# Kernel tuning notes

Hardware: AMD Instinct MI355X
Metric: run time of the kernel (lower is better)

The kernel has to match this reference:

```python
import jax, jax.numpy as jnp
import numpy as np

N = 100000   # active voxels (stride=1 -> output coords == input coords)
C_IN = 64
C_OUT = 64
K3 = 27      # 3x3x3 kernel offsets
M = 40000    # rulebook pairs per kernel offset
EPS = 1e-5


def setup_inputs() -> dict:
    key = jax.random.key(0)
    k1, k2, k3, k4 = jax.random.split(key, 4)
    x = jax.random.normal(k1, (N, C_IN), dtype=jnp.float32)
    # conv weights per kernel offset: [K3, inc, outc]
    W = jax.random.normal(k2, (K3, C_IN, C_OUT), dtype=jnp.float32) * 0.05
    gamma = jnp.ones((C_OUT,), dtype=jnp.float32)
    beta = jnp.zeros((C_OUT,), dtype=jnp.float32)
    # rulebook: for each offset k, M (input_idx, output_idx) pairs
    in_idx = jax.random.randint(k3, (K3, M), 0, N, dtype=jnp.int32)
    out_idx = jax.random.randint(k4, (K3, M), 0, N, dtype=jnp.int32)
    return {"x": x, "W": W, "gamma": gamma, "beta": beta,
            "in_idx": in_idx, "out_idx": out_idx}


def reference(x, W, gamma, beta, in_idx, out_idx):
    n_out = x.shape[0]  # stride=1: output voxel set == input voxel set
    # gather: [K3, M, C_IN]
    feat = x[in_idx]
    # batched GEMM over kernel offsets: [K3, M, C_OUT]
    contrib = jnp.einsum('kmi,kio->kmo', feat, W)
    # scatter-add into output voxels
    out = jnp.zeros((n_out, W.shape[2]), dtype=x.dtype)
    out = out.at[out_idx.reshape(-1)].add(contrib.reshape(-1, W.shape[2]))
    # BatchNorm over active points (training-mode batch stats, biased var)
    mean = jnp.mean(out, axis=0)
    var = jnp.mean(jnp.square(out - mean), axis=0)
    y = (out - mean) * jax.lax.rsqrt(var + EPS) * gamma + beta
    # ReLU
    return jnp.maximum(y, 0.0)
```

## Files before the change

kernel.cpp:

```cpp
#include <hip/hip_runtime.h>


#define N_VOX   100000
#define NPAD    100096
#define C_INCH  64
#define C_OUTCH 64
#define K3      27
#define M_PAIRS 40000
#define NPAIRS  (K3 * M_PAIRS)
#define BN_EPS  1e-5f
#define NBINS   (K3 * NPAD)
#define AUXMAX  184320
#define AUXCAP  (AUXMAX - 1)
#define ZROW    (N_VOX + AUXMAX - 1)
#define OVMAX   65536

#define OFF_WT     0u
#define OFF_STATS  221184u
#define OFF_CTRS   221696u
#define OFF_CNT    221760u
#define OFF_GINX   2924352u
#define OFF_IN1    13734720u
#define OFF_LIST   24545088u
#define OFF_OV     26019648u
#define OFF_XB     26543936u
#define WS_NEED    ((size_t)OFF_XB + (size_t)(N_VOX + AUXMAX) * 128u)

#define NB_WT 432
#define NB_XB 3125

typedef __attribute__((ext_vector_type(8))) short bf16x8;
typedef __attribute__((ext_vector_type(4))) float f32x4;

__device__ __forceinline__ short f2bf(float f) {
  unsigned u = __builtin_bit_cast(unsigned, f);
  u += 0x7FFFu + ((u >> 16) & 1u);
  return (short)(u >> 16);
}
__device__ __forceinline__ float bf2f(short s) {
  unsigned u = ((unsigned)(unsigned short)s) << 16;
  return __builtin_bit_cast(float, u);
}

__global__ __launch_bounds__(256) void init_kernel(const float* __restrict__ W,
                                                   const float* __restrict__ x,
                                                   short* __restrict__ wt,
                                                   short* __restrict__ xb) {
  int b = blockIdx.x, t = threadIdx.x;
  if (b < NB_WT) {
    int id = b * 256 + t;
    int k = id >> 12, rem = id & 4095, c = rem >> 6, i = rem & 63;
    wt[id] = f2bf(W[(k << 12) + (i << 6) + c]);
  } else if (b < NB_WT + NB_XB) {
    int id = (b - NB_WT) * 256 + t;
    if (id < N_VOX * 8) {
      float4 lo = ((const float4*)x)[id * 2];
      float4 hi = ((const float4*)x)[id * 2 + 1];
      bf16x8 v;
      v[0] = f2bf(lo.x); v[1] = f2bf(lo.y); v[2] = f2bf(lo.z); v[3] = f2bf(lo.w);
      v[4] = f2bf(hi.x); v[5] = f2bf(hi.y); v[6] = f2bf(hi.z); v[7] = f2bf(hi.w);
      ((bf16x8*)xb)[id] = v;
    }
  } else {
    if (t < 8) {
      bf16x8 z = {0, 0, 0, 0, 0, 0, 0, 0};
      ((bf16x8*)(xb + (size_t)ZROW * 64))[t] = z;
    }
  }
}

__global__ __launch_bounds__(256) void build_kernel(const int* __restrict__ in_idx,
                                                    const int* __restrict__ out_idx,
                                                    unsigned* __restrict__ cnt32,
                                                    int* __restrict__ ginx,
                                                    int* __restrict__ in1,
                                                    int2* __restrict__ ov,
                                                    int* __restrict__ ctrs) {
  __shared__ int l_cnt, l_base;
  int t = threadIdx.x;
  if (t == 0) l_cnt = 0;
  __syncthreads();
  int id = blockIdx.x * 256 + t;
  int lpos = -1;
  int2 entry = make_int2(0, 0);
  if (id < NPAIRS) {
    int k  = id / M_PAIRS;
    int in = in_idx[id];
    int o  = out_idx[id];
    int b  = k * NPAD + o;
    unsigned sh   = (unsigned)(b & 3) * 8u;
    unsigned old  = atomicAdd(&cnt32[b >> 2], 1u << sh);
    unsigned slot = (old >> sh) & 0xFFu;
    if (slot == 0u)      ginx[b] = in;
    else if (slot == 1u) in1[b]  = in;
    else { lpos = atomicAdd(&l_cnt, 1); entry = make_int2((k << 17) | in, o); }
  }
  __syncthreads();
  if (t == 0) l_base = (l_cnt > 0) ? atomicAdd(&ctrs[1], l_cnt) : 0;
  __syncthreads();
  if (lpos >= 0) {
    int p = l_base + lpos;
    if (p < OVMAX) ov[p] = entry;
  }
}

__global__ __launch_bounds__(256) void scan_kernel(const unsigned* __restrict__ cnt32,
                                                   int* __restrict__ ginx,
                                                   const int* __restrict__ in1,
                                                   int2* __restrict__ list,
                                                   int* __restrict__ ctrs) {
  __shared__ int l_cnt, l_base;
  int t = threadIdx.x;
  if (t == 0) l_cnt = 0;
  __syncthreads();
  int w = blockIdx.x * 256 + t;
  unsigned c4 = (w < NBINS / 4) ? cnt32[w] : 0u;
  int lp[4];
  #pragma unroll
  for (int s = 0; s < 4; ++s) {
    unsigned c = (c4 >> (s * 8)) & 0xFFu;
    lp[s] = (c >= 2u) ? atomicAdd(&l_cnt, 1) : -1;
  }
  __syncthreads();
  if (t == 0) l_base = (l_cnt > 0) ? atomicAdd(&ctrs[0], l_cnt) : 0;
  __syncthreads();
  int base = l_base;
  #pragma unroll
  for (int s = 0; s < 4; ++s) {
    if (lp[s] >= 0) {
      int b   = w * 4 + s;
      int pos = base + lp[s];
      if (pos < AUXCAP) {
        list[pos] = make_int2(ginx[b], in1[b]);
        ginx[b]   = N_VOX + pos;
      }
    }
  }
}

__global__ __launch_bounds__(256) void fixup_kernel(short* __restrict__ xb,
                                                    const int2* __restrict__ list,
                                                    const int* __restrict__ ctrs) {
  int n = ctrs[0]; if (n > AUXCAP) n = AUXCAP;
  int wid  = (blockIdx.x * 256 + threadIdx.x) >> 6;
  int lane = threadIdx.x & 63;
  int nw   = gridDim.x * 4;
  for (int i = wid; i < n; i += nw) {
    int2 p = list[i];
    float a = bf2f(xb[(size_t)p.x * 64 + lane]);
    float b = bf2f(xb[(size_t)p.y * 64 + lane]);
    xb[(size_t)(N_VOX + i) * 64 + lane] = f2bf(a + b);
  }
}

__global__ __launch_bounds__(256) void conv_out_kernel(const short* __restrict__ xb,
                                                       const short* __restrict__ wt,
                                                       const int* __restrict__ ginx,
                                                       float* __restrict__ out) {
  __shared__ short lds[2 * 4096];
  int t = threadIdx.x, wave = t >> 6, lane = t & 63;
  int g = lane >> 4, c0 = lane & 15, g8 = g * 8;
  int obase = blockIdx.x * 64 + wave * 16;
  int o = obase + c0;

  int rb  = ((c0 * 128 + g * 16) ^ ((c0 & 7) << 4)) >> 1;
  int wb0 = ((t * 32) ^ (((t >> 2) & 7) << 4)) >> 1;

  f32x4 acc[4];
  #pragma unroll
  for (int n = 0; n < 4; ++n) { acc[n][0]=0.f; acc[n][1]=0.f; acc[n][2]=0.f; acc[n][3]=0.f; }

  bf16x8 s0 = *(const bf16x8*)(wt + t * 16);
  bf16x8 s1 = *(const bf16x8*)(wt + t * 16 + 8);
  int i0 = ginx[o];        i0 = (i0 < 0) ? ZROW : i0;
  const short* xr0 = xb + (size_t)i0 * 64;
  bf16x8 a0c = *(const bf16x8*)(xr0 + g8);
  bf16x8 a1c = *(const bf16x8*)(xr0 + 32 + g8);
  int i1 = ginx[NPAD + o]; i1 = (i1 < 0) ? ZROW : i1;
  *(bf16x8*)&lds[wb0]     = s0;
  *(bf16x8*)&lds[wb0 ^ 8] = s1;
  __syncthreads();

  int buf = 0;
  for (int k = 0; k < K3; ++k) {
    if (k + 1 < K3) {
      const short* wn = wt + (size_t)(k + 1) * 4096 + t * 16;
      s0 = *(const bf16x8*)(wn);
      s1 = *(const bf16x8*)(wn + 8);
    }
    const short* xr = xb + (size_t)i1 * 64;
    bf16x8 a0n = *(const bf16x8*)(xr + g8);
    bf16x8 a1n = *(const bf16x8*)(xr + 32 + g8);
    int i2 = ZROW;
    if (k + 2 < K3) { int r = ginx[(size_t)(k + 2) * NPAD + o]; i2 = (r < 0) ? ZROW : r; }

    const short* lb = lds + buf * 4096;
    #pragma unroll
    for (int n = 0; n < 4; ++n) {
      bf16x8 b0 = *(const bf16x8*)&lb[rb + n * 1024];
      bf16x8 b1 = *(const bf16x8*)&lb[(rb ^ 32) + n * 1024];
      acc[n] = __builtin_amdgcn_mfma_f32_16x16x32_bf16(a0c, b0, acc[n], 0, 0, 0);
      acc[n] = __builtin_amdgcn_mfma_f32_16x16x32_bf16(a1c, b1, acc[n], 0, 0, 0);
    }
    if (k + 1 < K3) {
      short* wd = lds + (buf ^ 1) * 4096;
      *(bf16x8*)&wd[wb0]     = s0;
      *(bf16x8*)&wd[wb0 ^ 8] = s1;
    }
    __syncthreads();
    a0c = a0n; a1c = a1n; i1 = i2; buf ^= 1;
  }

  int orow = obase + (g << 2);
  #pragma unroll
  for (int j = 0; j < 4; ++j) {
    int r = orow + j;
    if (r < N_VOX) {
      float* op = out + (size_t)r * 64 + c0;
      op[0]  = acc[0][j];
      op[16] = acc[1][j];
      op[32] = acc[2][j];
      op[48] = acc[3][j];
    }
  }
}

__global__ __launch_bounds__(256) void ov_kernel(const float* __restrict__ x,
                                                 const float* __restrict__ W,
                                                 const int2* __restrict__ ov,
                                                 const int* __restrict__ ctrs,
                                                 float* __restrict__ out) {
  int n = ctrs[1]; if (n > OVMAX) n = OVMAX;
  int wid  = (blockIdx.x * 256 + threadIdx.x) >> 6;
  int lane = threadIdx.x & 63;
  int nw   = gridDim.x * 4;
  for (int i = wid; i < n; i += nw) {
    int2 e = ov[i];
    int in = e.x & 0x1FFFF;
    int k  = e.x >> 17;
    int o  = e.y;
    const float* xr = x + (size_t)in * 64;
    const float* wp = W + (size_t)k * 4096 + lane;
    float d = 0.f;
    #pragma unroll 8
    for (int ii = 0; ii < 64; ++ii) d += xr[ii] * wp[ii * 64];
    unsafeAtomicAdd(&out[(size_t)o * 64 + lane], d);
  }
}

__global__ __launch_bounds__(256) void conv_kernel(const float* __restrict__ x,
                                                   const short* __restrict__ wt,
                                                   const int* __restrict__ in_idx,
                                                   const int* __restrict__ out_idx,
                                                   float* __restrict__ out) {
  __shared__ int s_in[64];
  __shared__ int s_out[64];
  int bx = blockIdx.x;
  int k = bx / (M_PAIRS / 64), base = (bx % (M_PAIRS / 64)) * 64;
  int t = threadIdx.x;
  if (t < 64)       s_in[t]       = in_idx[k * M_PAIRS + base + t];
  else if (t < 128) s_out[t - 64] = out_idx[k * M_PAIRS + base + (t - 64)];
  __syncthreads();
  int wave = t >> 6, lane = t & 63, g = lane >> 4, c0 = lane & 15;
  const float* xrow = x + (size_t)s_in[(wave << 4) + c0] * C_INCH + g * 8;
  float4 a0lo = *(const float4*)(xrow);
  float4 a0hi = *(const float4*)(xrow + 4);
  float4 a1lo = *(const float4*)(xrow + 32);
  float4 a1hi = *(const float4*)(xrow + 36);
  bf16x8 a0, a1;
  a0[0]=f2bf(a0lo.x); a0[1]=f2bf(a0lo.y); a0[2]=f2bf(a0lo.z); a0[3]=f2bf(a0lo.w);
  a0[4]=f2bf(a0hi.x); a0[5]=f2bf(a0hi.y); a0[6]=f2bf(a0hi.z); a0[7]=f2bf(a0hi.w);
  a1[0]=f2bf(a1lo.x); a1[1]=f2bf(a1lo.y); a1[2]=f2bf(a1lo.z); a1[3]=f2bf(a1lo.w);
  a1[4]=f2bf(a1hi.x); a1[5]=f2bf(a1hi.y); a1[6]=f2bf(a1hi.z); a1[7]=f2bf(a1hi.w);
  const short* wtk = wt + k * 4096;
  f32x4 acc[4];
  #pragma unroll
  for (int n = 0; n < 4; ++n) { acc[n][0]=0.f; acc[n][1]=0.f; acc[n][2]=0.f; acc[n][3]=0.f; }
  #pragma unroll
  for (int n = 0; n < 4; ++n) {
    int c = n * 16 + c0;
    bf16x8 b0 = *(const bf16x8*)(wtk + c * 64 + g * 8);
    bf16x8 b1 = *(const bf16x8*)(wtk + c * 64 + 32 + g * 8);
    acc[n] = __builtin_amdgcn_mfma_f32_16x16x32_bf16(a0, b0, acc[n], 0, 0, 0);
    acc[n] = __builtin_amdgcn_mfma_f32_16x16x32_bf16(a1, b1, acc[n], 0, 0, 0);
  }
  int rbase = (wave << 4) + ((lane >> 4) << 2);
  #pragma unroll
  for (int j = 0; j < 4; ++j) {
    size_t o2 = (size_t)s_out[rbase + j] * C_OUTCH;
    #pragma unroll
    for (int n = 0; n < 4; ++n) unsafeAtomicAdd(&out[o2 + n * 16 + c0], acc[n][j]);
  }
}

__global__ __launch_bounds__(256) void stats_kernel(const float* __restrict__ out,
                                                    float* __restrict__ stats) {
  __shared__ float s1[256], s2[256];
  int t = threadIdx.x, c = t & 63, rsub = t >> 6;
  float sum1 = 0.f, sum2 = 0.f;
  for (int r = blockIdx.x * 4 + rsub; r < N_VOX; r += gridDim.x * 4) {
    float v = out[r * 64 + c];
    sum1 += v; sum2 += v * v;
  }
  s1[t] = sum1; s2[t] = sum2;
  __syncthreads();
  if (t < 64) {
    sum1 = s1[t] + s1[t + 64] + s1[t + 128] + s1[t + 192];
    sum2 = s2[t] + s2[t + 64] + s2[t + 128] + s2[t + 192];
    unsafeAtomicAdd(&stats[c], sum1);
    unsafeAtomicAdd(&stats[64 + c], sum2);
  }
}

__global__ __launch_bounds__(256) void norm_kernel(float* __restrict__ out,
                                                   const float* __restrict__ stats,
                                                   const float* __restrict__ gamma,
                                                   const float* __restrict__ beta) {
  int i4 = blockIdx.x * 256 + threadIdx.x;
  if (i4 >= N_VOX * (C_OUTCH / 4)) return;
  const float invN = 1.0f / (float)N_VOX;
  float4 v = ((const float4*)out)[i4];
  int c0 = (i4 << 2) & 63;
  float r[4] = {v.x, v.y, v.z, v.w};
  #pragma unroll
  for (int j = 0; j < 4; ++j) {
    int c = c0 + j;
    float mean = stats[c] * invN;
    float ex2  = stats[64 + c] * invN;
    float var  = ex2 - mean * mean;
    float scale = gamma[c] * rsqrtf(var + BN_EPS);
    float shift = beta[c] - mean * scale;
    r[j] = fmaxf(r[j] * scale + shift, 0.0f);
  }
  v.x = r[0]; v.y = r[1]; v.z = r[2]; v.w = r[3];
  ((float4*)out)[i4] = v;
}

extern "C" void kernel_launch(void* const* d_in, const int* in_sizes, int n_in,
                              void* d_out, int out_size, void* d_ws, size_t ws_size,
                              hipStream_t stream) {
  const float* x      = (const float*)d_in[0];
  const float* W      = (const float*)d_in[1];
  const float* gamma  = (const float*)d_in[2];
  const float* beta   = (const float*)d_in[3];
  const int*   in_idx = (const int*)d_in[4];
  const int*   out_idx= (const int*)d_in[5];
  float* out = (float*)d_out;

  char* ws = (char*)d_ws;
  short*    wt    = (short*)(ws + OFF_WT);
  float*    stats = (float*)(ws + OFF_STATS);
  int*      ctrs  = (int*)(ws + OFF_CTRS);
  unsigned* cnt32 = (unsigned*)(ws + OFF_CNT);
  int*      ginx  = (int*)(ws + OFF_GINX);
  int*      in1   = (int*)(ws + OFF_IN1);
  int2*     list  = (int2*)(ws + OFF_LIST);
  int2*     ov    = (int2*)(ws + OFF_OV);
  short*    xb    = (short*)(ws + OFF_XB);

  hipMemsetAsync(ws + OFF_STATS, 0, OFF_CNT - OFF_STATS, stream);

  if (ws_size >= WS_NEED) {
    hipMemsetAsync(ws + OFF_CNT, 0x00, NBINS, stream);
    hipMemsetAsync(ws + OFF_GINX, 0xFF, NBINS * 4, stream);
    init_kernel<<<NB_WT + NB_XB + 1, 256, 0, stream>>>(W, x, wt, xb);
    build_kernel<<<(NPAIRS + 255) / 256, 256, 0, stream>>>(in_idx, out_idx,
                                                           cnt32, ginx, in1, ov, ctrs);
    scan_kernel<<<(NBINS / 4 + 255) / 256, 256, 0, stream>>>(cnt32, ginx, in1, list, ctrs);
    fixup_kernel<<<2048, 256, 0, stream>>>(xb, list, ctrs);
    conv_out_kernel<<<NPAD / 64, 256, 0, stream>>>(xb, wt, ginx, out);
    ov_kernel<<<1024, 256, 0, stream>>>(x, W, ov, ctrs, out);
  } else {
    init_kernel<<<NB_WT + NB_XB + 1, 256, 0, stream>>>(W, x, wt, xb);
    hipMemsetAsync(d_out, 0, (size_t)N_VOX * C_OUTCH * sizeof(float), stream);
    conv_kernel<<<K3 * (M_PAIRS / 64), 256, 0, stream>>>(x, wt, in_idx, out_idx, out);
  }

  stats_kernel<<<512, 256, 0, stream>>>(out, stats);
  norm_kernel<<<(N_VOX * (C_OUTCH / 4) + 255) / 256, 256, 0, stream>>>(out, stats, gamma, beta);
}
```

Baseline: 266.7 us.

## Replace count-based rulebook binning with linked lists and fuse BN stats into conv

Output-stationary binning now uses atomicExch-built linked lists per (offset, output) bin, so bins with any number of pairs are pre-summed in the fixup kernel. This removes the separate fp32 overflow kernel with its atomics, and the extra count and in1 arrays. The conv kernel now processes 128 outputs per block (two 16-row tiles per wave), reusing each LDS weight fragment across both tiles. It also accumulates BatchNorm sum and sum-of-squares directly, which drops the separate stats pass over the output. The cost is a fixup kernel that chases pointer chains, plus higher register pressure in conv.

```diff
diff --git a/kernel.cpp b/kernel.cpp
--- a/kernel.cpp
+++ b/kernel.cpp
@@ -13,17 +13,14 @@
 #define AUXMAX  184320
 #define AUXCAP  (AUXMAX - 1)
 #define ZROW    (N_VOX + AUXMAX - 1)
-#define OVMAX   65536
 
 #define OFF_WT     0u
 #define OFF_STATS  221184u
 #define OFF_CTRS   221696u
-#define OFF_CNT    221760u
-#define OFF_GINX   2924352u
-#define OFF_IN1    13734720u
-#define OFF_LIST   24545088u
-#define OFF_OV     26019648u
-#define OFF_XB     26543936u
+#define OFF_BING   221760u
+#define OFF_NODE   11032128u
+#define OFF_LIST   19672128u
+#define OFF_XB     20409472u
 #define WS_NEED    ((size_t)OFF_XB + (size_t)(N_VOX + AUXMAX) * 128u)
 
 #define NB_WT 432
@@ -71,181 +68,179 @@
 
 __global__ __launch_bounds__(256) void build_kernel(const int* __restrict__ in_idx,
                                                     const int* __restrict__ out_idx,
-                                                    unsigned* __restrict__ cnt32,
-                                                    int* __restrict__ ginx,
-                                                    int* __restrict__ in1,
-                                                    int2* __restrict__ ov,
-                                                    int* __restrict__ ctrs) {
+                                                    int* __restrict__ bing,
+                                                    int2* __restrict__ node) {
+  int id = blockIdx.x * 256 + threadIdx.x;
+  if (id >= NPAIRS) return;
+  int k  = id / M_PAIRS;
+  int in = in_idx[id];
+  int o  = out_idx[id];
+  int b  = k * NPAD + o;
+  int old = atomicExch(&bing[b], id);
+  node[id] = make_int2(old, in);
+}
+
+__global__ __launch_bounds__(256) void compact_kernel(int* __restrict__ bing,
+                                                      const int2* __restrict__ node,
+                                                      int* __restrict__ list,
+                                                      int* __restrict__ ctrs) {
   __shared__ int l_cnt, l_base;
   int t = threadIdx.x;
   if (t == 0) l_cnt = 0;
   __syncthreads();
-  int id = blockIdx.x * 256 + t;
-  int lpos = -1;
-  int2 entry = make_int2(0, 0);
-  if (id < NPAIRS) {
-    int k  = id / M_PAIRS;
-    int in = in_idx[id];
-    int o  = out_idx[id];
-    int b  = k * NPAD + o;
-    unsigned sh   = (unsigned)(b & 3) * 8u;
-    unsigned old  = atomicAdd(&cnt32[b >> 2], 1u << sh);
-    unsigned slot = (old >> sh) & 0xFFu;
-    if (slot == 0u)      ginx[b] = in;
-    else if (slot == 1u) in1[b]  = in;
-    else { lpos = atomicAdd(&l_cnt, 1); entry = make_int2((k << 17) | in, o); }
-  }
-  __syncthreads();
-  if (t == 0) l_base = (l_cnt > 0) ? atomicAdd(&ctrs[1], l_cnt) : 0;
-  __syncthreads();
-  if (lpos >= 0) {
-    int p = l_base + lpos;
-    if (p < OVMAX) ov[p] = entry;
-  }
-}
-
-__global__ __launch_bounds__(256) void scan_kernel(const unsigned* __restrict__ cnt32,
-                                                   int* __restrict__ ginx,
-                                                   const int* __restrict__ in1,
-                                                   int2* __restrict__ list,
-                                                   int* __restrict__ ctrs) {
-  __shared__ int l_cnt, l_base;
-  int t = threadIdx.x;
-  if (t == 0) l_cnt = 0;
-  __syncthreads();
   int w = blockIdx.x * 256 + t;
-  unsigned c4 = (w < NBINS / 4) ? cnt32[w] : 0u;
+  bool ok = (w < NBINS / 4);
+  int4 h4 = ok ? ((int4*)bing)[w] : make_int4(-1, -1, -1, -1);
+  int hv[4] = {h4.x, h4.y, h4.z, h4.w};
+  int gv[4];
   int lp[4];
+  int2 n0[4];
   #pragma unroll
   for (int s = 0; s < 4; ++s) {
-    unsigned c = (c4 >> (s * 8)) & 0xFFu;
-    lp[s] = (c >= 2u) ? atomicAdd(&l_cnt, 1) : -1;
+    lp[s] = -1;
+    if (hv[s] < 0) { gv[s] = ZROW; }
+    else {
+      n0[s] = node[hv[s]];
+      if (n0[s].x < 0) gv[s] = n0[s].y;
+      else             lp[s] = atomicAdd(&l_cnt, 1);
+    }
   }
   __syncthreads();
   if (t == 0) l_base = (l_cnt > 0) ? atomicAdd(&ctrs[0], l_cnt) : 0;
   __syncthreads();
-  int base = l_base;
   #pragma unroll
   for (int s = 0; s < 4; ++s) {
     if (lp[s] >= 0) {
-      int b   = w * 4 + s;
-      int pos = base + lp[s];
-      if (pos < AUXCAP) {
-        list[pos] = make_int2(ginx[b], in1[b]);
-        ginx[b]   = N_VOX + pos;
-      }
-    }
-  }
+      int pos = l_base + lp[s];
+      if (pos < AUXCAP) { list[pos] = hv[s]; gv[s] = N_VOX + pos; }
+      else              { gv[s] = n0[s].y; }
+    }
+  }
+  if (ok) ((int4*)bing)[w] = make_int4(gv[0], gv[1], gv[2], gv[3]);
 }
 
 __global__ __launch_bounds__(256) void fixup_kernel(short* __restrict__ xb,
-                                                    const int2* __restrict__ list,
+                                                    const int* __restrict__ list,
+                                                    const int2* __restrict__ node,
                                                     const int* __restrict__ ctrs) {
   int n = ctrs[0]; if (n > AUXCAP) n = AUXCAP;
   int wid  = (blockIdx.x * 256 + threadIdx.x) >> 6;
   int lane = threadIdx.x & 63;
   int nw   = gridDim.x * 4;
   for (int i = wid; i < n; i += nw) {
-    int2 p = list[i];
-    float a = bf2f(xb[(size_t)p.x * 64 + lane]);
-    float b = bf2f(xb[(size_t)p.y * 64 + lane]);
-    xb[(size_t)(N_VOX + i) * 64 + lane] = f2bf(a + b);
+    int h = list[i];
+    float acc = 0.f;
+    while (h >= 0) {
+      int2 nd = node[h];
+      acc += bf2f(xb[(size_t)nd.y * 64 + lane]);
+      h = nd.x;
+    }
+    xb[(size_t)(N_VOX + i) * 64 + lane] = f2bf(acc);
   }
 }
 
 __global__ __launch_bounds__(256) void conv_out_kernel(const short* __restrict__ xb,
                                                        const short* __restrict__ wt,
-                                                       const int* __restrict__ ginx,
-                                                       float* __restrict__ out) {
+                                                       const int* __restrict__ bing,
+                                                       float* __restrict__ out,
+                                                       float* __restrict__ stats) {
   __shared__ short lds[2 * 4096];
+  __shared__ float ls[128];
   int t = threadIdx.x, wave = t >> 6, lane = t & 63;
   int g = lane >> 4, c0 = lane & 15, g8 = g * 8;
-  int obase = blockIdx.x * 64 + wave * 16;
-  int o = obase + c0;
+  int o0 = blockIdx.x * 128 + wave * 32 + c0;
+  int o1 = o0 + 16;
 
   int rb  = ((c0 * 128 + g * 16) ^ ((c0 & 7) << 4)) >> 1;
   int wb0 = ((t * 32) ^ (((t >> 2) & 7) << 4)) >> 1;
-
-  f32x4 acc[4];
-  #pragma unroll
-  for (int n = 0; n < 4; ++n) { acc[n][0]=0.f; acc[n][1]=0.f; acc[n][2]=0.f; acc[n][3]=0.f; }
-
-  bf16x8 s0 = *(const bf16x8*)(wt + t * 16);
-  bf16x8 s1 = *(const bf16x8*)(wt + t * 16 + 8);
-  int i0 = ginx[o];        i0 = (i0 < 0) ? ZROW : i0;
-  const short* xr0 = xb + (size_t)i0 * 64;
-  bf16x8 a0c = *(const bf16x8*)(xr0 + g8);
-  bf16x8 a1c = *(const bf16x8*)(xr0 + 32 + g8);
-  int i1 = ginx[NPAD + o]; i1 = (i1 < 0) ? ZROW : i1;
-  *(bf16x8*)&lds[wb0]     = s0;
-  *(bf16x8*)&lds[wb0 ^ 8] = s1;
+  if (t < 128) ls[t] = 0.f;
+
+  f32x4 acc0[4], acc1[4];
+  #pragma unroll
+  for (int n = 0; n < 4; ++n) {
+    acc0[n][0]=0.f; acc0[n][1]=0.f; acc0[n][2]=0.f; acc0[n][3]=0.f;
+    acc1[n][0]=0.f; acc1[n][1]=0.f; acc1[n][2]=0.f; acc1[n][3]=0.f;
+  }
+
+  bf16x8 s0w = *(const bf16x8*)(wt + t * 16);
+  bf16x8 s1w = *(const bf16x8*)(wt + t * 16 + 8);
+  int ia = bing[o0], ib = bing[o1];
+  const short* xa = xb + (size_t)ia * 64;
+  const short* xc = xb + (size_t)ib * 64;
+  bf16x8 a0c = *(const bf16x8*)(xa + g8);
+  bf16x8 a1c = *(const bf16x8*)(xa + 32 + g8);
+  bf16x8 a2c = *(const bf16x8*)(xc + g8);
+  bf16x8 a3c = *(const bf16x8*)(xc + 32 + g8);
+  int i1a = bing[NPAD + o0], i1b = bing[NPAD + o1];
+  *(bf16x8*)&lds[wb0]     = s0w;
+  *(bf16x8*)&lds[wb0 ^ 8] = s1w;
   __syncthreads();
 
   int buf = 0;
   for (int k = 0; k < K3; ++k) {
     if (k + 1 < K3) {
       const short* wn = wt + (size_t)(k + 1) * 4096 + t * 16;
-      s0 = *(const bf16x8*)(wn);
-      s1 = *(const bf16x8*)(wn + 8);
-    }
-    const short* xr = xb + (size_t)i1 * 64;
-    bf16x8 a0n = *(const bf16x8*)(xr + g8);
-    bf16x8 a1n = *(const bf16x8*)(xr + 32 + g8);
-    int i2 = ZROW;
-    if (k + 2 < K3) { int r = ginx[(size_t)(k + 2) * NPAD + o]; i2 = (r < 0) ? ZROW : r; }
-
+      s0w = *(const bf16x8*)(wn);
+      s1w = *(const bf16x8*)(wn + 8);
+    }
+    const short* pa = xb + (size_t)i1a * 64;
+    const short* pb = xb + (size_t)i1b * 64;
+    bf16x8 a0n = *(const bf16x8*)(pa + g8);
+    bf16x8 a1n = *(const bf16x8*)(pa + 32 + g8);
+    bf16x8 a2n = *(const bf16x8*)(pb + g8);
+    bf16x8 a3n = *(const bf16x8*)(pb + 32 + g8);
+    int i2a = ZROW, i2b = ZROW;
+    if (k + 2 < K3) {
+      i2a = bing[(size_t)(k + 2) * NPAD + o0];
+      i2b = bing[(size_t)(k + 2) * NPAD + o1];
+    }
     const short* lb = lds + buf * 4096;
     #pragma unroll
     for (int n = 0; n < 4; ++n) {
       bf16x8 b0 = *(const bf16x8*)&lb[rb + n * 1024];
       bf16x8 b1 = *(const bf16x8*)&lb[(rb ^ 32) + n * 1024];
-      acc[n] = __builtin_amdgcn_mfma_f32_16x16x32_bf16(a0c, b0, acc[n], 0, 0, 0);
-      acc[n] = __builtin_amdgcn_mfma_f32_16x16x32_bf16(a1c, b1, acc[n], 0, 0, 0);
+      acc0[n] = __builtin_amdgcn_mfma_f32_16x16x32_bf16(a0c, b0, acc0[n], 0, 0, 0);
+      acc0[n] = __builtin_amdgcn_mfma_f32_16x16x32_bf16(a1c, b1, acc0[n], 0, 0, 0);
+      acc1[n] = __builtin_amdgcn_mfma_f32_16x16x32_bf16(a2c, b0, acc1[n], 0, 0, 0);
+      acc1[n] = __builtin_amdgcn_mfma_f32_16x16x32_bf16(a3c, b1, acc1[n], 0, 0, 0);
     }
     if (k + 1 < K3) {
       short* wd = lds + (buf ^ 1) * 4096;
-      *(bf16x8*)&wd[wb0]     = s0;
-      *(bf16x8*)&wd[wb0 ^ 8] = s1;
+      *(bf16x8*)&wd[wb0]     = s0w;
+      *(bf16x8*)&wd[wb0 ^ 8] = s1w;
     }
     __syncthreads();
-    a0c = a0n; a1c = a1n; i1 = i2; buf ^= 1;
-  }
-
-  int orow = obase + (g << 2);
+    a0c = a0n; a1c = a1n; a2c = a2n; a3c = a3n;
+    i1a = i2a; i1b = i2b; buf ^= 1;
+  }
+
+  int orow = blockIdx.x * 128 + wave * 32 + (g << 2);
   #pragma unroll
   for (int j = 0; j < 4; ++j) {
-    int r = orow + j;
-    if (r < N_VOX) {
-      float* op = out + (size_t)r * 64 + c0;
-      op[0]  = acc[0][j];
-      op[16] = acc[1][j];
-      op[32] = acc[2][j];
-      op[48] = acc[3][j];
-    }
-  }
-}
-
-__global__ __launch_bounds__(256) void ov_kernel(const float* __restrict__ x,
-                                                 const float* __restrict__ W,
-                                                 const int2* __restrict__ ov,
-                                                 const int* __restrict__ ctrs,
-                                                 float* __restrict__ out) {
-  int n = ctrs[1]; if (n > OVMAX) n = OVMAX;
-  int wid  = (blockIdx.x * 256 + threadIdx.x) >> 6;
-  int lane = threadIdx.x & 63;
-  int nw   = gridDim.x * 4;
-  for (int i = wid; i < n; i += nw) {
-    int2 e = ov[i];
-    int in = e.x & 0x1FFFF;
-    int k  = e.x >> 17;
-    int o  = e.y;
-    const float* xr = x + (size_t)in * 64;
-    const float* wp = W + (size_t)k * 4096 + lane;
-    float d = 0.f;
-    #pragma unroll 8
-    for (int ii = 0; ii < 64; ++ii) d += xr[ii] * wp[ii * 64];
-    unsafeAtomicAdd(&out[(size_t)o * 64 + lane], d);
-  }
+    int r0 = orow + j, r1 = orow + 16 + j;
+    if (r0 < N_VOX) {
+      float* op = out + (size_t)r0 * 64 + c0;
+      op[0] = acc0[0][j]; op[16] = acc0[1][j]; op[32] = acc0[2][j]; op[48] = acc0[3][j];
+    }
+    if (r1 < N_VOX) {
+      float* op = out + (size_t)r1 * 64 + c0;
+      op[0] = acc1[0][j]; op[16] = acc1[1][j]; op[32] = acc1[2][j]; op[48] = acc1[3][j];
+    }
+  }
+
+  #pragma unroll
+  for (int n = 0; n < 4; ++n) {
+    float s = 0.f, q = 0.f;
+    #pragma unroll
+    for (int j = 0; j < 4; ++j) {
+      float v0 = acc0[n][j], v1 = acc1[n][j];
+      s += v0 + v1; q += v0 * v0 + v1 * v1;
+    }
+    atomicAdd(&ls[n * 16 + c0], s);
+    atomicAdd(&ls[64 + n * 16 + c0], q);
+  }
+  __syncthreads();
+  if (t < 128) unsafeAtomicAdd(&stats[t], ls[t]);
 }
 
 __global__ __launch_bounds__(256) void conv_kernel(const float* __restrict__ x,
@@ -348,34 +343,29 @@
   float* out = (float*)d_out;
 
   char* ws = (char*)d_ws;
-  short*    wt    = (short*)(ws + OFF_WT);
-  float*    stats = (float*)(ws + OFF_STATS);
-  int*      ctrs  = (int*)(ws + OFF_CTRS);
-  unsigned* cnt32 = (unsigned*)(ws + OFF_CNT);
-  int*      ginx  = (int*)(ws + OFF_GINX);
-  int*      in1   = (int*)(ws + OFF_IN1);
-  int2*     list  = (int2*)(ws + OFF_LIST);
-  int2*     ov    = (int2*)(ws + OFF_OV);
-  short*    xb    = (short*)(ws + OFF_XB);
-
-  hipMemsetAsync(ws + OFF_STATS, 0, OFF_CNT - OFF_STATS, stream);
+  short* wt    = (short*)(ws + OFF_WT);
+  float* stats = (float*)(ws + OFF_STATS);
+  int*   ctrs  = (int*)(ws + OFF_CTRS);
+  int*   bing  = (int*)(ws + OFF_BING);
+  int2*  node  = (int2*)(ws + OFF_NODE);
+  int*   list  = (int*)(ws + OFF_LIST);
+  short* xb    = (short*)(ws + OFF_XB);
+
+  hipMemsetAsync(ws + OFF_STATS, 0, OFF_BING - OFF_STATS, stream);
 
   if (ws_size >= WS_NEED) {
-    hipMemsetAsync(ws + OFF_CNT, 0x00, NBINS, stream);
-    hipMemsetAsync(ws + OFF_GINX, 0xFF, NBINS * 4, stream);
+    hipMemsetAsync(ws + OFF_BING, 0xFF, NBINS * 4, stream);
     init_kernel<<<NB_WT + NB_XB + 1, 256, 0, stream>>>(W, x, wt, xb);
-    build_kernel<<<(NPAIRS + 255) / 256, 256, 0, stream>>>(in_idx, out_idx,
-                                                           cnt32, ginx, in1, ov, ctrs);
-    scan_kernel<<<(NBINS / 4 + 255) / 256, 256, 0, stream>>>(cnt32, ginx, in1, list, ctrs);
-    fixup_kernel<<<2048, 256, 0, stream>>>(xb, list, ctrs);
-    conv_out_kernel<<<NPAD / 64, 256, 0, stream>>>(xb, wt, ginx, out);
-    ov_kernel<<<1024, 256, 0, stream>>>(x, W, ov, ctrs, out);
+    build_kernel<<<(NPAIRS + 255) / 256, 256, 0, stream>>>(in_idx, out_idx, bing, node);
+    compact_kernel<<<(NBINS / 4 + 255) / 256, 256, 0, stream>>>(bing, node, list, ctrs);
+    fixup_kernel<<<2048, 256, 0, stream>>>(xb, list, node, ctrs);
+    conv_out_kernel<<<NPAD / 128, 256, 0, stream>>>(xb, wt, bing, out, stats);
   } else {
     init_kernel<<<NB_WT + NB_XB + 1, 256, 0, stream>>>(W, x, wt, xb);
     hipMemsetAsync(d_out, 0, (size_t)N_VOX * C_OUTCH * sizeof(float), stream);
     conv_kernel<<<K3 * (M_PAIRS / 64), 256, 0, stream>>>(x, wt, in_idx, out_idx, out);
-  }
-
-  stats_kernel<<<512, 256, 0, stream>>>(out, stats);
+    stats_kernel<<<512, 256, 0, stream>>>(out, stats);
+  }
+
   norm_kernel<<<(N_VOX * (C_OUTCH / 4) + 255) / 256, 256, 0, stream>>>(out, stats, gamma, beta);
 }
```

Measured after the change: 218.6 us. 18.0% less time.
